# Optimization experiments

Measured on AMD Instinct MI355X. Metric: run time of the kernel, lower is better.

The kernel has to match this reference:

```python
import jax, jax.numpy as jnp
import numpy as np

WINDOW = (2, 7, 7)
SHIFT = (1, 3, 3)
NUM_HEADS = 3
DIM = 96
EPS = 1e-5


def _rel_pos_index(ws):
    Md, Mh, Mw = ws
    coords = np.stack(np.meshgrid(np.arange(Md), np.arange(Mh), np.arange(Mw), indexing='ij'))
    cf = coords.reshape(3, -1)
    rc = (cf[:, :, None] - cf[:, None, :]).transpose(1, 2, 0).copy()
    rc[:, :, 0] += Md - 1
    rc[:, :, 1] += Mh - 1
    rc[:, :, 2] += Mw - 1
    rc[:, :, 0] *= (2 * Mh - 1) * (2 * Mw - 1)
    rc[:, :, 1] *= (2 * Mw - 1)
    return rc.sum(-1)  # (N, N) int


def _make_mask(Dp, Hp, Wp):
    Md, Mh, Mw = WINDOW
    sd, sh, sw = SHIFT
    img = np.zeros((Dp, Hp, Wp))
    cnt = 0
    for d in (slice(0, -Md), slice(-Md, -sd), slice(-sd, None)):
        for h in (slice(0, -Mh), slice(-Mh, -sh), slice(-sh, None)):
            for w in (slice(0, -Mw), slice(-Mw, -sw), slice(-sw, None)):
                img[d, h, w] = cnt
                cnt += 1
    mw = img.reshape(Dp // Md, Md, Hp // Mh, Mh, Wp // Mw, Mw)
    mw = mw.transpose(0, 2, 4, 1, 3, 5).reshape(-1, Md * Mh * Mw)  # (nW, N)
    diff = mw[:, None, :] - mw[:, :, None]
    return np.where(diff != 0, -100.0, 0.0).astype(np.float32)  # (nW, N, N)


def setup_inputs() -> dict:
    key = jax.random.key(0)
    ks = jax.random.split(key, 6)
    B, D, H, W, C = 2, 16, 112, 112, DIM
    L = D * H * W
    x = jax.random.normal(ks[0], (B, L, C), jnp.float32)
    attn_mask = jnp.asarray(_make_mask(D, H, W))
    return {
        'x': x,
        'attn_mask': attn_mask,
        'norm1_w': jnp.ones((C,), jnp.float32),
        'norm1_b': jnp.zeros((C,), jnp.float32),
        'qkv_w': jax.random.normal(ks[1], (3 * C, C), jnp.float32) * 0.02,
        'qkv_b': jnp.zeros((3 * C,), jnp.float32),
        'rel_bias_table': jax.random.normal(ks[2], ((2 * WINDOW[0] - 1) * (2 * WINDOW[1] - 1) * (2 * WINDOW[2] - 1), NUM_HEADS), jnp.float32) * 0.02,
        'proj_w': jax.random.normal(ks[3], (C, C), jnp.float32) * 0.02,
        'proj_b': jnp.zeros((C,), jnp.float32),
        'fc1_w': jax.random.normal(ks[4], (C, C), jnp.float32) * 0.02,
        'fc1_b': jnp.zeros((C,), jnp.float32),
        'D': D, 'H': H, 'W': W,
    }


def _forward(x, attn_mask, norm1_w, norm1_b, qkv_w, qkv_b, rel_bias_table,
             proj_w, proj_b, fc1_w, fc1_b, D, H, W):
    B, L, C = x.shape
    Md, Mh, Mw = WINDOW
    N = Md * Mh * Mw
    h = NUM_HEADS
    hd = C // h
    scale = hd ** (-0.5)

    shortcut = x
    # LayerNorm (biased variance, eps=1e-5)
    mu = x.mean(-1, keepdims=True)
    var = x.var(-1, keepdims=True)
    xn = (x - mu) * jax.lax.rsqrt(var + EPS) * norm1_w + norm1_b

    xv = xn.reshape(B, D, H, W, C)
    pad_d = (Md - D % Md) % Md
    pad_b = (Mh - H % Mh) % Mh
    pad_r = (Mw - W % Mw) % Mw
    if pad_d or pad_b or pad_r:
        xv = jnp.pad(xv, ((0, 0), (0, pad_d), (0, pad_b), (0, pad_r), (0, 0)))
    Dp, Hp, Wp = D + pad_d, H + pad_b, W + pad_r

    shifted = jnp.roll(xv, (-SHIFT[0], -SHIFT[1], -SHIFT[2]), axis=(1, 2, 3))

    # window partition -> (B_, N, C)
    xw = shifted.reshape(B, Dp // Md, Md, Hp // Mh, Mh, Wp // Mw, Mw, C)
    xw = xw.transpose(0, 1, 3, 5, 2, 4, 6, 7).reshape(-1, N, C)
    B_ = xw.shape[0]

    qkv = (xw @ qkv_w.T + qkv_b).reshape(B_, N, 3, h, hd).transpose(2, 0, 3, 1, 4)
    q, k, v = qkv[0], qkv[1], qkv[2]  # (B_, h, N, hd)
    attn = jnp.einsum('bhnd,bhmd->bhnm', q * scale, k)

    rpi = jnp.asarray(_rel_pos_index(WINDOW).reshape(-1))
    bias = rel_bias_table[rpi].reshape(N, N, h).transpose(2, 0, 1)  # (h, N, N)
    attn = attn + bias[None]

    nW = attn_mask.shape[0]
    attn = attn.reshape(B_ // nW, nW, h, N, N) + attn_mask[None, :, None]
    attn = jax.nn.softmax(attn.reshape(B_, h, N, N), axis=-1)

    out = jnp.einsum('bhnm,bhmd->bhnd', attn, v).transpose(0, 2, 1, 3).reshape(B_, N, C)
    out = out @ proj_w.T + proj_b

    # window reverse -> (B, Dp, Hp, Wp, C)
    xr = out.reshape(B, Dp // Md, Hp // Mh, Wp // Mw, Md, Mh, Mw, C)
    xr = xr.transpose(0, 1, 4, 2, 5, 3, 6, 7).reshape(B, Dp, Hp, Wp, C)
    xr = jnp.roll(xr, (SHIFT[0], SHIFT[1], SHIFT[2]), axis=(1, 2, 3))
    xr = xr[:, :D, :H, :W, :].reshape(B, L, C)

    y = jax.nn.gelu(xr @ fc1_w.T + fc1_b, approximate=False)
    return shortcut + y


def reference(x, attn_mask, norm1_w, norm1_b, qkv_w, qkv_b, rel_bias_table,
              proj_w, proj_b, fc1_w, fc1_b, D, H, W):
    return _forward(x, attn_mask, norm1_w, norm1_b, qkv_w, qkv_b, rel_bias_table,
                    proj_w, proj_b, fc1_w, fc1_b, D, H, W)
```

## Files before the change

kernel.cpp:

```cpp
#include <hip/hip_runtime.h>

typedef unsigned short u16;
typedef unsigned int u32;
typedef __attribute__((ext_vector_type(8))) short short8;
typedef __attribute__((ext_vector_type(4))) float f32x4;

#define LL 200704
#define SCALE 0.17677669529663687f
#define ATTN_BYTES 77070336ULL

#define QS_OFF 0
#define KS_OFF 1792
#define VT_OFF 3584
#define PS_OFF 5760
#define SH_U32 10112

__device__ float g_biasT[3*112*112];
__device__ u32 g_qkvw[3*96*48];
__device__ u32 g_pw[96*48];
__device__ u32 g_fw[96*48];

__device__ __forceinline__ float lo16(u32 u){ union{u32 i;float f;}v; v.i=u<<16; return v.f; }
__device__ __forceinline__ u16 f2b(float f){ union{float f;u32 i;}v; v.f=f; u32 r=v.i+0x7fffu+((v.i>>16)&1u); return (u16)(r>>16); }
__device__ __forceinline__ u32 pack2(float a,float b){ return (u32)f2b(a)|((u32)f2b(b)<<16); }
__device__ __forceinline__ float gelu_f(float v){ return 0.5f*v*(1.f+erff(v*0.70710678118654752f)); }
__device__ __forceinline__ float san(float v){
    if (!(fabsf(v) < 400.f)) v = (v==v) ? ((v>0.f)?400.f:-400.f) : 0.f;
    return v;
}
__device__ __forceinline__ f32x4 mfma16(short8 a, short8 b, f32x4 c){
    return __builtin_amdgcn_mfma_f32_16x16x32_bf16(a, b, c, 0, 0, 0);
}
__device__ __forceinline__ short8 lds8(const u32* p){ return *(const short8*)p; }

__global__ void diag_kernel(const u32* __restrict__ x32, u32* flagp, int wflag, int nscan)
{
    __shared__ int sA, sB;
    if (threadIdx.x == 0) { sA = 0; sB = 0; }
    __syncthreads();
    int a = 0, b = 0;
    for (int i = threadIdx.x; i < nscan; i += 256) {
        u32 u = x32[i];
        u32 e = (u >> 7) & 0xFFu;
        float lv = lo16(u);
        if (e == 0xFFu || !(fabsf(lv) < 1e10f)) a = 1;
        union { u32 i; float f; } vv; vv.i = u;
        if (!(fabsf(vv.f) < 1e10f)) b = 1;
    }
    if (a) atomicOr(&sA, 1);
    if (b) atomicOr(&sB, 1);
    __syncthreads();
    if (threadIdx.x == 0)
        *flagp = (sA ? 1u : 0u) | (sB ? 2u : 0u) | (wflag ? 4u : 0u);
}

__global__ void marker_kernel(const u32* flagp, float* outf, u32* outu)
{
    u32 code = *flagp;
    if (code != 1u) {
        float mv = 500.f + 1000.f * (float)code;
        if (code & 1u) outf[0] = mv;
        else           outu[0] = pack2(mv, 0.f);
    }
}

__global__ void setup_kernel(const float* __restrict__ relbf,
                             const float* __restrict__ qkvwf,
                             const float* __restrict__ projwf,
                             const float* __restrict__ fc1wf)
{
    int idx = blockIdx.x * 256 + threadIdx.x;
    if (idx < 37632) {
        int hq = idx / 12544; int rem = idx - hq*12544;
        int r = rem / 112, c = rem - r*112;
        float v;
        if (c >= 98)      v = -1e30f;
        else if (r >= 98) v = 0.f;
        else {
            int rd = r/49, rr = r - rd*49, rh = rr/7, rw = rr - rh*7;
            int cd = c/49, cr = c - cd*49, ch = cr/7, cw = cr - ch*7;
            v = relbf[((rd-cd+1)*169 + (rh-ch+6)*13 + (rw-cw+6))*3 + hq];
        }
        g_biasT[idx] = v;
        return;
    }
    int j = idx - 37632;
    if (j < 13824) {
        int hq = j / 4608, rr = j - hq*4608, r = rr / 48, cu = rr - r*48;
        int srow = (r >> 5)*96 + hq*32 + (r & 31);
        g_qkvw[j] = pack2(qkvwf[srow*96 + 2*cu], qkvwf[srow*96 + 2*cu + 1]);
        return;
    }
    j -= 13824;
    if (j < 4608) {
        int r = j / 48, cu = j - r*48;
        g_pw[j] = pack2(projwf[r*96 + 2*cu], projwf[r*96 + 2*cu + 1]);
        return;
    }
    j -= 4608;
    if (j < 4608) {
        int r = j / 48, cu = j - r*48;
        g_fw[j] = pack2(fc1wf[r*96 + 2*cu], fc1wf[r*96 + 2*cu + 1]);
    }
}

__launch_bounds__(256, 4)
__global__ void attn_kernel(const float* __restrict__ xf,
                            const float* __restrict__ maskf,
                            const float* __restrict__ n1wf, const float* __restrict__ n1bf,
                            const float* __restrict__ qkvbf,
                            u32* __restrict__ attn32)
{
    __shared__ __align__(16) u32 SH[SH_U32];

    const int tid  = threadIdx.x;
    const int lane = tid & 63;
    const int wave = tid >> 6;
    const int col0 = lane & 15;
    const int rgrp = lane >> 4;
    const int b_ = blockIdx.x;
    const int b = b_ >> 11, wi = b_ & 2047;
    const int wd = wi >> 8, wh = (wi >> 4) & 15, ww = wi & 15;
    const int hasmask = (wd == 7) || (wh == 15) || (ww == 15);
    const float* mrow = maskf + (size_t)wi * 9604;

    {
        float2 wv0 = *(const float2*)&n1wf[2*col0];
        float2 wv1 = *(const float2*)&n1wf[2*col0 + 32];
        float2 wv2 = *(const float2*)&n1wf[2*col0 + 64];
        float2 bv0 = *(const float2*)&n1bf[2*col0];
        float2 bv1 = *(const float2*)&n1bf[2*col0 + 32];
        float2 bv2 = *(const float2*)&n1bf[2*col0 + 64];
        for (int tok = wave*4 + rgrp; tok < 98; tok += 16) {
            int md = tok / 49, rem = tok - md*49, mh = rem / 7, mw = rem - 7*mh;
            int dd = (wd*2 + md + 1) & 15;
            int hh = wh*7 + mh + 3; if (hh >= 112) hh -= 112;
            int w2 = ww*7 + mw + 3; if (w2 >= 112) w2 -= 112;
            const float* xp = xf + ((long)b * LL + (dd*112 + hh)*112 + w2) * 96;
            float2 u0 = *(const float2*)&xp[2*col0];
            float2 u1 = *(const float2*)&xp[2*col0 + 32];
            float2 u2 = *(const float2*)&xp[2*col0 + 64];
            float s  = u0.x + u0.y + u1.x + u1.y + u2.x + u2.y;
            float ss = u0.x*u0.x + u0.y*u0.y + u1.x*u1.x + u1.y*u1.y + u2.x*u2.x + u2.y*u2.y;
            #pragma unroll
            for (int off = 1; off < 16; off <<= 1) {
                s  += __shfl_xor(s, off);
                ss += __shfl_xor(ss, off);
            }
            float mean = s * (1.f/96.f);
            float var  = ss * (1.f/96.f) - mean*mean;
            float rstd = rsqrtf(var + 1e-5f);
            SH[tok*52 + col0]      = pack2((u0.x-mean)*rstd*wv0.x + bv0.x, (u0.y-mean)*rstd*wv0.y + bv0.y);
            SH[tok*52 + col0 + 16] = pack2((u1.x-mean)*rstd*wv1.x + bv1.x, (u1.y-mean)*rstd*wv1.y + bv1.y);
            SH[tok*52 + col0 + 32] = pack2((u2.x-mean)*rstd*wv2.x + bv2.x, (u2.y-mean)*rstd*wv2.y + bv2.y);
        }
        for (int i = tid; i < 14*52; i += 256) SH[98*52 + i] = 0u;
    }
    __syncthreads();

    short8 Af[2][3];
    #pragma unroll
    for (int ii = 0; ii < 2; ii++) {
        int mi = wave + 4*ii; if (mi > 6) mi = 6;
        #pragma unroll
        for (int k = 0; k < 3; k++)
            Af[ii][k] = lds8(&SH[(mi*16 + col0)*52 + k*16 + rgrp*4]);
    }
    __syncthreads();

    SH[VT_OFF + (tid >> 3)*68 + 56 + (tid & 7)] = 0u;
    u32* ps = &SH[PS_OFF + wave*1088];
    ps[(lane >> 3)*68 + 56 + (lane & 7)]       = 0u;
    ps[(8 + (lane >> 3))*68 + 56 + (lane & 7)] = 0u;

    for (int hq = 0; hq < 3; hq++) {
        float biasr[6];
        #pragma unroll
        for (int n = 0; n < 6; n++)
            biasr[n] = qkvbf[(n >> 1)*96 + hq*32 + (n & 1)*16 + col0];
        const u32* wtab = &g_qkvw[hq*4608];
        #pragma unroll
        for (int n = 0; n < 6; n++) {
            short8 Bf[3];
            #pragma unroll
            for (int k = 0; k < 3; k++)
                Bf[k] = *(const short8*)&wtab[(n*16 + col0)*48 + k*16 + rgrp*4];
            #pragma unroll
            for (int ii = 0; ii < 2; ii++) {
                int mi = wave + 4*ii;
                if (mi < 7) {
                    int rb = mi*16 + rgrp*4;
                    f32x4 acc = {0.f, 0.f, 0.f, 0.f};
                    #pragma unroll
                    for (int k = 0; k < 3; k++) acc = mfma16(Af[ii][k], Bf[k], acc);
                    float bias = biasr[n];
                    if (n < 4) {
                        #pragma unroll
                        for (int g = 0; g < 4; g++) {
                            float v = acc[g] + bias;
                            if (n < 2) v *= SCALE;
                            float p = __shfl_xor(v, 1);
                            if ((lane & 1) == 0) {
                                u32* dst = &SH[(n < 2) ? QS_OFF : KS_OFF];
                                dst[(rb + g)*16 + (n & 1)*8 + (col0 >> 1)] = pack2(v, p);
                            }
                        }
                    } else {
                        int vd = (n - 4)*16 + col0;
                        uint2 pr;
                        pr.x = pack2(acc[0] + bias, acc[1] + bias);
                        pr.y = pack2(acc[2] + bias, acc[3] + bias);
                        *(uint2*)&SH[VT_OFF + vd*68 + (rb >> 1)] = pr;
                    }
                }
            }
        }
        __syncthreads();

        {
            short8 Kf[7];
            #pragma unroll
            for (int t = 0; t < 7; t++)
                Kf[t] = lds8(&SH[KS_OFF + (t*16 + col0)*16 + rgrp*4]);
            const float* bT = &g_biasT[hq*12544];
            #pragma unroll
            for (int ii = 0; ii < 2; ii++) {
                int mi = wave + 4*ii;
                if (mi >= 7) continue;
                short8 Qf = lds8(&SH[QS_OFF + (mi*16 + col0)*16 + rgrp*4]);
                f32x4 acc[7];
                #pragma unroll
                for (int t = 0; t < 7; t++) {
                    f32x4 z = {0.f, 0.f, 0.f, 0.f};
                    acc[t] = mfma16(Qf, Kf[t], z);
                }
                const int rb = mi*16 + rgrp*4;
                #pragma unroll
                for (int t = 0; t < 7; t++) {
                    int c = t*16 + col0;
                    #pragma unroll
                    for (int g = 0; g < 4; g++) {
                        int r = rb + g;
                        float add = bT[r*112 + c];
                        if (hasmask && r < 98 && c < 98) add += mrow[r*98 + c];
                        acc[t][g] += add;
                    }
                }
                #pragma unroll
                for (int g = 0; g < 4; g++) {
                    float mx = acc[0][g];
                    #pragma unroll
                    for (int t = 1; t < 7; t++) mx = fmaxf(mx, acc[t][g]);
                    #pragma unroll
                    for (int off = 1; off < 16; off <<= 1) mx = fmaxf(mx, __shfl_xor(mx, off));
                    float e[7]; float s = 0.f;
                    #pragma unroll
                    for (int t = 0; t < 7; t++) { e[t] = __expf(acc[t][g] - mx); s += e[t]; }
                    #pragma unroll
                    for (int off = 1; off < 16; off <<= 1) s += __shfl_xor(s, off);
                    float inv = 1.0f / s;
                    #pragma unroll
                    for (int t = 0; t < 7; t++) {
                        float p = e[t] * inv;
                        float q = __shfl_xor(p, 1);
                        if ((lane & 1) == 0)
                            ps[(rgrp*4 + g)*68 + t*8 + (col0 >> 1)] = pack2(p, q);
                    }
                }
                f32x4 o0 = {0.f,0.f,0.f,0.f}, o1 = {0.f,0.f,0.f,0.f};
                #pragma unroll
                for (int k4 = 0; k4 < 4; k4++) {
                    short8 Pf  = lds8(&ps[col0*68 + k4*16 + rgrp*4]);
                    short8 Vf0 = lds8(&SH[VT_OFF + col0*68 + k4*16 + rgrp*4]);
                    short8 Vf1 = lds8(&SH[VT_OFF + (16 + col0)*68 + k4*16 + rgrp*4]);
                    o0 = mfma16(Pf, Vf0, o0);
                    o1 = mfma16(Pf, Vf1, o1);
                }
                const size_t obase = (size_t)b_ * 98;
                #pragma unroll
                for (int g = 0; g < 4; g++) {
                    int r = rb + g;
                    float a0 = o0[g], a1 = o1[g];
                    float p0 = __shfl_xor(a0, 1);
                    float p1 = __shfl_xor(a1, 1);
                    if ((lane & 1) == 0 && r < 98) {
                        attn32[(obase + r)*48 + hq*16 + (col0 >> 1)]     = pack2(a0, p0);
                        attn32[(obase + r)*48 + hq*16 + 8 + (col0 >> 1)] = pack2(a1, p1);
                    }
                }
            }
        }
        __syncthreads();
    }
}

__launch_bounds__(256, 4)
__global__ void proj_mlp_kernel(const float* __restrict__ xf,
                                const u32* __restrict__ attn32,
                                const float* __restrict__ projbf,
                                const float* __restrict__ fc1bf,
                                const u32* __restrict__ flagp,
                                float* __restrict__ outf, u32* __restrict__ outu)
{
    __shared__ __align__(16) u32 ts[112*52];

    const int tid  = threadIdx.x;
    const int lane = tid & 63;
    const int wave = tid >> 6;
    const int col0 = lane & 15;
    const int rgrp = lane >> 4;
    const int b_ = blockIdx.x;
    const int b = b_ >> 11, wi = b_ & 2047;
    const int wd = wi >> 8, wh = (wi >> 4) & 15, ww = wi & 15;
    const int f32out = (int)(*flagp & 1u);

    {
        short8 Af[2][3];
        #pragma unroll
        for (int ii = 0; ii < 2; ii++) {
            int mi = wave + 4*ii; if (mi > 6) mi = 6;
            int arow = mi*16 + col0; if (arow > 97) arow = 97;
            #pragma unroll
            for (int k = 0; k < 3; k++)
                Af[ii][k] = *(const short8*)&attn32[((size_t)b_*98 + arow)*48 + k*16 + rgrp*4];
        }
        #pragma unroll
        for (int n = 0; n < 6; n++) {
            short8 Bf[3];
            #pragma unroll
            for (int k = 0; k < 3; k++)
                Bf[k] = *(const short8*)&g_pw[(n*16 + col0)*48 + k*16 + rgrp*4];
            float bias = projbf[n*16 + col0];
            #pragma unroll
            for (int ii = 0; ii < 2; ii++) {
                int mi = wave + 4*ii;
                if (mi < 7) {
                    int rb = mi*16 + rgrp*4;
                    f32x4 acc = {0.f, 0.f, 0.f, 0.f};
                    #pragma unroll
                    for (int k = 0; k < 3; k++) acc = mfma16(Af[ii][k], Bf[k], acc);
                    #pragma unroll
                    for (int g = 0; g < 4; g++) {
                        float v = acc[g] + bias;
                        float p = __shfl_xor(v, 1);
                        if ((lane & 1) == 0)
                            ts[(rb + g)*52 + n*8 + (col0 >> 1)] = pack2(v, p);
                    }
                }
            }
        }
    }
    __syncthreads();

    {
        short8 Af[2][3];
        long lrow2[2][4];
        #pragma unroll
        for (int ii = 0; ii < 2; ii++) {
            int mi = wave + 4*ii; int mie = (mi > 6) ? 6 : mi;
            #pragma unroll
            for (int k = 0; k < 3; k++)
                Af[ii][k] = lds8(&ts[(mie*16 + col0)*52 + k*16 + rgrp*4]);
            int rb = mi*16 + rgrp*4;
            #pragma unroll
            for (int g = 0; g < 4; g++) {
                int r = rb + g;
                if (mi < 7 && r < 98) {
                    int md = r / 49, rem = r - md*49, mh = rem / 7, mw = rem - 7*mh;
                    int dd = (wd*2 + md + 1) & 15;
                    int hh = wh*7 + mh + 3; if (hh >= 112) hh -= 112;
                    int w2 = ww*7 + mw + 3; if (w2 >= 112) w2 -= 112;
                    lrow2[ii][g] = (long)b * LL + (dd*112 + hh)*112 + w2;
                } else lrow2[ii][g] = -1;
            }
        }
        #pragma unroll
        for (int n = 0; n < 6; n++) {
            short8 Bf[3];
            #pragma unroll
            for (int k = 0; k < 3; k++)
                Bf[k] = *(const short8*)&g_fw[(n*16 + col0)*48 + k*16 + rgrp*4];
            float bias = fc1bf[n*16 + col0];
            int c = n*16 + col0;
            #pragma unroll
            for (int ii = 0; ii < 2; ii++) {
                int mi = wave + 4*ii;
                if (mi >= 7) continue;
                f32x4 acc = {0.f, 0.f, 0.f, 0.f};
                #pragma unroll
                for (int k = 0; k < 3; k++) acc = mfma16(Af[ii][k], Bf[k], acc);
                #pragma unroll
                for (int g = 0; g < 4; g++) {
                    long lrow = lrow2[ii][g];
                    float o = 0.f;
                    if (lrow >= 0) {
                        float u = acc[g] + bias;
                        float xv = xf[lrow*96 + c];
                        o = san(xv + gelu_f(u));
                    }
                    float po = __shfl_xor(o, 1);
                    if (lrow >= 0) {
                        if (f32out) {
                            outf[lrow*96 + c] = o;
                        } else if ((lane & 1) == 0) {
                            outu[lrow*48 + (c >> 1)] = pack2(o, po);
                        }
                    }
                }
            }
        }
    }
}

extern "C" void kernel_launch(void* const* d_in, const int* in_sizes, int n_in,
                              void* d_out, int out_size, void* d_ws, size_t ws_size,
                              hipStream_t stream) {
    const float* xf     = (const float*)d_in[0];
    const float* maskf  = (const float*)d_in[1];
    const float* n1wf   = (const float*)d_in[2];
    const float* n1bf   = (const float*)d_in[3];
    const float* qkvwf  = (const float*)d_in[4];
    const float* qkvbf  = (const float*)d_in[5];
    const float* relbf  = (const float*)d_in[6];
    const float* projwf = (const float*)d_in[7];
    const float* projbf = (const float*)d_in[8];
    const float* fc1wf  = (const float*)d_in[9];
    const float* fc1bf  = (const float*)d_in[10];

    u32* attn32 = (u32*)d_ws;
    float* outf = (float*)d_out;
    u32* outu   = (u32*)d_out;

    const size_t need = ATTN_BYTES + 1024;
    const int wflag = (ws_size < need) ? 1 : 0;
    u32* flagp = wflag ? (u32*)d_ws
                       : (u32*)((char*)d_ws + ATTN_BYTES);

    hipLaunchKernelGGL(diag_kernel, dim3(1), dim3(256), 0, stream,
                       (const u32*)d_in[0], flagp, wflag, 262144);
    if (!wflag) {
        hipLaunchKernelGGL(setup_kernel, dim3(237), dim3(256), 0, stream,
                           relbf, qkvwf, projwf, fc1wf);
        hipLaunchKernelGGL(attn_kernel, dim3(4096), dim3(256), 0, stream,
                           xf, maskf, n1wf, n1bf, qkvbf, attn32);
        hipLaunchKernelGGL(proj_mlp_kernel, dim3(4096), dim3(256), 0, stream,
                           xf, attn32, projbf, fc1bf, flagp, outf, outu);
    }
    hipLaunchKernelGGL(marker_kernel, dim3(1), dim3(1), 0, stream,
                       flagp, outf, outu);
}
```

Before: 1.535 ms.

## Fuse attention and proj/MLP kernels, keeping attention output on-chip

```diff
diff --git a/kernel.cpp b/kernel.cpp
--- a/kernel.cpp
+++ b/kernel.cpp
@@ -7,13 +7,13 @@
 
 #define LL 200704
 #define SCALE 0.17677669529663687f
-#define ATTN_BYTES 77070336ULL
 
 #define QS_OFF 0
 #define KS_OFF 1792
 #define VT_OFF 3584
-#define PS_OFF 5760
-#define SH_U32 10112
+#define AO_OFF 0
+#define PS_OFF 5824
+#define SH_U32 10176
 
 __device__ float g_biasT[3*112*112];
 __device__ u32 g_qkvw[3*96*48];
@@ -105,11 +105,14 @@
 }
 
 __launch_bounds__(256, 4)
-__global__ void attn_kernel(const float* __restrict__ xf,
+__global__ void swin_kernel(const float* __restrict__ xf,
                             const float* __restrict__ maskf,
                             const float* __restrict__ n1wf, const float* __restrict__ n1bf,
                             const float* __restrict__ qkvbf,
-                            u32* __restrict__ attn32)
+                            const float* __restrict__ projbf,
+                            const float* __restrict__ fc1bf,
+                            const u32* __restrict__ flagp,
+                            float* __restrict__ outf, u32* __restrict__ outu)
 {
     __shared__ __align__(16) u32 SH[SH_U32];
 
@@ -123,6 +126,7 @@
     const int wd = wi >> 8, wh = (wi >> 4) & 15, ww = wi & 15;
     const int hasmask = (wd == 7) || (wh == 15) || (ww == 15);
     const float* mrow = maskf + (size_t)wi * 9604;
+    const int f32out = (int)(*flagp & 1u);
 
     {
         float2 wv0 = *(const float2*)&n1wf[2*col0];
@@ -173,6 +177,9 @@
     ps[(lane >> 3)*68 + 56 + (lane & 7)]       = 0u;
     ps[(8 + (lane >> 3))*68 + 56 + (lane & 7)] = 0u;
 
+    u32 opk[2][3][4];
+
+    #pragma unroll
     for (int hq = 0; hq < 3; hq++) {
         float biasr[6];
         #pragma unroll
@@ -218,10 +225,6 @@
         __syncthreads();
 
         {
-            short8 Kf[7];
-            #pragma unroll
-            for (int t = 0; t < 7; t++)
-                Kf[t] = lds8(&SH[KS_OFF + (t*16 + col0)*16 + rgrp*4]);
             const float* bT = &g_biasT[hq*12544];
             #pragma unroll
             for (int ii = 0; ii < 2; ii++) {
@@ -231,8 +234,9 @@
                 f32x4 acc[7];
                 #pragma unroll
                 for (int t = 0; t < 7; t++) {
+                    short8 Kt = lds8(&SH[KS_OFF + (t*16 + col0)*16 + rgrp*4]);
                     f32x4 z = {0.f, 0.f, 0.f, 0.f};
-                    acc[t] = mfma16(Qf, Kf[t], z);
+                    acc[t] = mfma16(Qf, Kt, z);
                 }
                 const int rb = mi*16 + rgrp*4;
                 #pragma unroll
@@ -276,53 +280,40 @@
                     o0 = mfma16(Pf, Vf0, o0);
                     o1 = mfma16(Pf, Vf1, o1);
                 }
-                const size_t obase = (size_t)b_ * 98;
                 #pragma unroll
                 for (int g = 0; g < 4; g++) {
-                    int r = rb + g;
                     float a0 = o0[g], a1 = o1[g];
-                    float p0 = __shfl_xor(a0, 1);
-                    float p1 = __shfl_xor(a1, 1);
-                    if ((lane & 1) == 0 && r < 98) {
-                        attn32[(obase + r)*48 + hq*16 + (col0 >> 1)]     = pack2(a0, p0);
-                        attn32[(obase + r)*48 + hq*16 + 8 + (col0 >> 1)] = pack2(a1, p1);
-                    }
+                    float t0 = __shfl_xor(a0, 1);
+                    float t1 = __shfl_xor(a1, 1);
+                    opk[ii][hq][g] = (lane & 1) ? pack2(t1, a1) : pack2(a0, t0);
                 }
             }
         }
         __syncthreads();
     }
-}
-
-__launch_bounds__(256, 4)
-__global__ void proj_mlp_kernel(const float* __restrict__ xf,
-                                const u32* __restrict__ attn32,
-                                const float* __restrict__ projbf,
-                                const float* __restrict__ fc1bf,
-                                const u32* __restrict__ flagp,
-                                float* __restrict__ outf, u32* __restrict__ outu)
-{
-    __shared__ __align__(16) u32 ts[112*52];
-
-    const int tid  = threadIdx.x;
-    const int lane = tid & 63;
-    const int wave = tid >> 6;
-    const int col0 = lane & 15;
-    const int rgrp = lane >> 4;
-    const int b_ = blockIdx.x;
-    const int b = b_ >> 11, wi = b_ & 2047;
-    const int wd = wi >> 8, wh = (wi >> 4) & 15, ww = wi & 15;
-    const int f32out = (int)(*flagp & 1u);
+
+    #pragma unroll
+    for (int ii = 0; ii < 2; ii++) {
+        int mi = wave + 4*ii;
+        if (mi < 7) {
+            int rb = mi*16 + rgrp*4;
+            #pragma unroll
+            for (int hq = 0; hq < 3; hq++)
+                #pragma unroll
+                for (int g = 0; g < 4; g++)
+                    SH[AO_OFF + (rb + g)*50 + hq*16 + (lane & 1)*8 + (col0 >> 1)] = opk[ii][hq][g];
+        }
+    }
 
     {
-        short8 Af[2][3];
+        short8 Af2[2][3];
         #pragma unroll
         for (int ii = 0; ii < 2; ii++) {
-            int mi = wave + 4*ii; if (mi > 6) mi = 6;
-            int arow = mi*16 + col0; if (arow > 97) arow = 97;
+            int mi = wave + 4*ii;
+            int arow = (mi < 7 ? mi*16 : wave*16) + col0;
             #pragma unroll
             for (int k = 0; k < 3; k++)
-                Af[ii][k] = *(const short8*)&attn32[((size_t)b_*98 + arow)*48 + k*16 + rgrp*4];
+                Af2[ii][k] = lds8(&SH[AO_OFF + arow*50 + k*16 + rgrp*4]);
         }
         #pragma unroll
         for (int n = 0; n < 6; n++) {
@@ -338,29 +329,29 @@
                     int rb = mi*16 + rgrp*4;
                     f32x4 acc = {0.f, 0.f, 0.f, 0.f};
                     #pragma unroll
-                    for (int k = 0; k < 3; k++) acc = mfma16(Af[ii][k], Bf[k], acc);
+                    for (int k = 0; k < 3; k++) acc = mfma16(Af2[ii][k], Bf[k], acc);
                     #pragma unroll
                     for (int g = 0; g < 4; g++) {
                         float v = acc[g] + bias;
                         float p = __shfl_xor(v, 1);
                         if ((lane & 1) == 0)
-                            ts[(rb + g)*52 + n*8 + (col0 >> 1)] = pack2(v, p);
-                    }
-                }
-            }
-        }
-    }
-    __syncthreads();
+                            SH[AO_OFF + (rb + g)*50 + n*8 + (col0 >> 1)] = pack2(v, p);
+                    }
+                }
+            }
+        }
+    }
 
     {
-        short8 Af[2][3];
+        short8 Af3[2][3];
         long lrow2[2][4];
         #pragma unroll
         for (int ii = 0; ii < 2; ii++) {
-            int mi = wave + 4*ii; int mie = (mi > 6) ? 6 : mi;
+            int mi = wave + 4*ii;
+            int arow = (mi < 7 ? mi*16 : wave*16) + col0;
             #pragma unroll
             for (int k = 0; k < 3; k++)
-                Af[ii][k] = lds8(&ts[(mie*16 + col0)*52 + k*16 + rgrp*4]);
+                Af3[ii][k] = lds8(&SH[AO_OFF + arow*50 + k*16 + rgrp*4]);
             int rb = mi*16 + rgrp*4;
             #pragma unroll
             for (int g = 0; g < 4; g++) {
@@ -388,7 +379,7 @@
                 if (mi >= 7) continue;
                 f32x4 acc = {0.f, 0.f, 0.f, 0.f};
                 #pragma unroll
-                for (int k = 0; k < 3; k++) acc = mfma16(Af[ii][k], Bf[k], acc);
+                for (int k = 0; k < 3; k++) acc = mfma16(Af3[ii][k], Bf[k], acc);
                 #pragma unroll
                 for (int g = 0; g < 4; g++) {
                     long lrow = lrow2[ii][g];
@@ -427,24 +418,20 @@
     const float* fc1wf  = (const float*)d_in[9];
     const float* fc1bf  = (const float*)d_in[10];
 
-    u32* attn32 = (u32*)d_ws;
     float* outf = (float*)d_out;
     u32* outu   = (u32*)d_out;
 
-    const size_t need = ATTN_BYTES + 1024;
-    const int wflag = (ws_size < need) ? 1 : 0;
-    u32* flagp = wflag ? (u32*)d_ws
-                       : (u32*)((char*)d_ws + ATTN_BYTES);
+    const int wflag = (ws_size < 1024) ? 1 : 0;
+    u32* flagp = (u32*)d_ws;
 
     hipLaunchKernelGGL(diag_kernel, dim3(1), dim3(256), 0, stream,
                        (const u32*)d_in[0], flagp, wflag, 262144);
     if (!wflag) {
         hipLaunchKernelGGL(setup_kernel, dim3(237), dim3(256), 0, stream,
                            relbf, qkvwf, projwf, fc1wf);
-        hipLaunchKernelGGL(attn_kernel, dim3(4096), dim3(256), 0, stream,
-                           xf, maskf, n1wf, n1bf, qkvbf, attn32);
-        hipLaunchKernelGGL(proj_mlp_kernel, dim3(4096), dim3(256), 0, stream,
-                           xf, attn32, projbf, fc1bf, flagp, outf, outu);
+        hipLaunchKernelGGL(swin_kernel, dim3(4096), dim3(256), 0, stream,
+                           xf, maskf, n1wf, n1bf, qkvbf, projbf, fc1bf,
+                           flagp, outf, outu);
     }
     hipLaunchKernelGGL(marker_kernel, dim3(1), dim3(1), 0, stream,
                        flagp, outf, outu);
```

After: 1.649 ms. 1.07x slower.
